# Kernel tuning notes

Measured on AMD Instinct MI355X. Metric: run time of the kernel, lower is better.

Reference implementation:

```python
import jax, jax.numpy as jnp
import numpy as np

N = 262144          # flattened node batch
IN_S, IN_V = 256, 32
OUT_S, OUT_V = 256, 32
H = max(IN_V, OUT_V)  # 32
EPS = 1e-4


def setup_inputs() -> dict:
    key = jax.random.key(0)
    ks = jax.random.split(key, 8)
    inv = lambda f: 1.0 / np.sqrt(f).astype(np.float32)
    return {
        "s": jax.random.normal(ks[0], (N, IN_S), jnp.float32),
        "V": jax.random.normal(ks[1], (N, IN_V, 3), jnp.float32),
        "W_h": jax.random.normal(ks[2], (H, IN_V), jnp.float32) * inv(IN_V),
        "W_mu": jax.random.normal(ks[3], (OUT_V, H), jnp.float32) * inv(H),
        "W_m_w": jax.random.normal(ks[4], (OUT_S, H + IN_S), jnp.float32) * inv(H + IN_S),
        "W_m_b": jax.random.normal(ks[5], (OUT_S,), jnp.float32) * 0.01,
        "W_g_w": jax.random.normal(ks[6], (OUT_V, OUT_S), jnp.float32) * inv(OUT_S),
        "W_g_b": jax.random.normal(ks[7], (OUT_V,), jnp.float32) * 0.01,
    }


def reference(s, V, W_h, W_mu, W_m_w, W_m_b, W_g_w, W_g_b):
    # V_h = W_h @ V : [N, H, 3]
    V_h = jnp.einsum('hv,nvc->nhc', W_h, V)
    # per-row L2 norm, clipped at eps : [N, H]
    s_h = jnp.maximum(jnp.linalg.norm(V_h, axis=-1), EPS)
    # Linear on concatenated scalars : [N, OUT_S]
    s_m = jnp.concatenate([s, s_h], axis=-1) @ W_m_w.T + W_m_b
    s_dash = jax.nn.relu(s_m)                      # sigma = relu
    # V_mu = W_mu @ V_h : [N, OUT_V, 3]
    V_mu = jnp.einsum('mh,nhc->nmc', W_mu, V_h)
    # vector gate: sigmoid(W_g(sigmoid(s_m)))  (sigma_plus = sigmoid)
    gate = jax.nn.sigmoid(jax.nn.sigmoid(s_m) @ W_g_w.T + W_g_b)  # [N, OUT_V]
    V_dash = gate[..., None] * V_mu
    return s_dash, V_dash
```

## Files before the change

### kernel.cpp

```cpp
#include <hip/hip_runtime.h>

#define NTOT 262144
#define BN   32
#define NT   256
#define SXS  296
#define VTS  36

typedef __attribute__((ext_vector_type(8))) short bf16x8;
typedef __attribute__((ext_vector_type(4))) float f32x4;

static __device__ __forceinline__ unsigned short f2b(float x) {
    union { float f; unsigned u; } c; c.f = x;
    unsigned r = c.u + 0x7FFFu + ((c.u >> 16) & 1u);
    return (unsigned short)(r >> 16);
}
static __device__ __forceinline__ float b2f(unsigned short h) {
    union { unsigned u; float f; } c; c.u = ((unsigned)h) << 16; return c.f;
}
static __device__ __forceinline__ bf16x8 cvt8(const float* p) {
    float4 x = *(const float4*)p, y = *(const float4*)(p + 4);
    bf16x8 r;
    r[0] = (short)f2b(x.x); r[1] = (short)f2b(x.y); r[2] = (short)f2b(x.z); r[3] = (short)f2b(x.w);
    r[4] = (short)f2b(y.x); r[5] = (short)f2b(y.y); r[6] = (short)f2b(y.z); r[7] = (short)f2b(y.w);
    return r;
}
static __device__ __forceinline__ void glds16(const unsigned short* g, void* l) {
    __builtin_amdgcn_global_load_lds(
        (const __attribute__((address_space(1))) void*)g,
        (__attribute__((address_space(3))) void*)l, 16, 0, 0);
}

__global__ void pack_w(const float* __restrict__ Wmw, const float* __restrict__ Wgw,
                       unsigned short* __restrict__ wp) {
    int t = blockIdx.x * 256 + threadIdx.x;
    if (t < 73728) {
        int o = t / 288, k = t % 288;
        int kks = (k & 31) ^ (((o >> 1) & 3) << 3);
        wp[(k >> 5) * 8192 + o * 32 + kks] = f2b(Wmw[t]);
    } else if (t < 81920) {
        int j = t - 73728;
        int o = j >> 8, k = j & 255;
        wp[73728 + (k >> 5) * 1024 + o * 32 + (k & 31)] = f2b(Wgw[j]);
    }
}

template<int USE_WS>
__global__ __launch_bounds__(NT, 2)
void gvp_main(const float* __restrict__ s, const float* __restrict__ V,
              const float* __restrict__ Wh, const float* __restrict__ Wmu,
              const float* __restrict__ Wmw, const float* __restrict__ Wmb,
              const float* __restrict__ Wgw, const float* __restrict__ Wgb,
              const unsigned short* __restrict__ wpack,
              float* __restrict__ out)
{
    __shared__ __attribute__((aligned(16))) unsigned short sX[BN * SXS];
    __shared__ __attribute__((aligned(16))) unsigned short sWb[2 * 8192];
    __shared__ __attribute__((aligned(16))) unsigned short sVT[96 * VTS];

    const int t  = threadIdx.x;
    const int w  = t >> 6, l = t & 63;
    const int fr = l & 15, fq = l >> 4;
    const int n0 = blockIdx.x * BN;
    const int half = w & 1, oh = w >> 1;

    if (USE_WS) {
        #pragma unroll
        for (int i = 0; i < 4; ++i)
            glds16(wpack + (w * 4 + i) * 512 + l * 8,
                   (char*)sWb + (w * 4 + i) * 1024);
    }

    #pragma unroll
    for (int i = 0; i < 8; ++i) {
        int n = i * 4 + w;
        float4 x4 = *(const float4*)&s[(size_t)(n0 + n) * 256 + 4 * l];
        ushort4 h4; h4.x = f2b(x4.x); h4.y = f2b(x4.y); h4.z = f2b(x4.z); h4.w = f2b(x4.w);
        *(ushort4*)&sX[n * SXS + 4 * l] = h4;
    }
    #pragma unroll
    for (int i = 0; i < 3; ++i) {
        int f = i * NT + t;
        float4 v4 = *(const float4*)&V[(size_t)n0 * 96 + f * 4];
        #pragma unroll
        for (int e = 0; e < 4; ++e) {
            int g = f * 4 + e;
            int n = g / 96, rem = g % 96, v = rem / 3, c = rem % 3;
            float val = (e == 0) ? v4.x : (e == 1) ? v4.y : (e == 2) ? v4.z : v4.w;
            sVT[(c * 32 + n) * VTS + v] = f2b(val);
        }
    }
    if (!USE_WS) {
        const float* p = &Wmw[t * 288];
        #pragma unroll
        for (int j = 0; j < 4; ++j)
            *(bf16x8*)&sWb[t * 32 + ((j ^ ((t >> 1) & 3)) << 3)] = cvt8(p + j * 8);
    }
    __syncthreads();

    {
        bf16x8 bh = cvt8(&Wh[(oh * 16 + fr) * 32 + fq * 8]);
        f32x4 va0 = {0,0,0,0}, va1 = {0,0,0,0}, va2 = {0,0,0,0};
        bf16x8 a0 = *(const bf16x8*)&sVT[(0 * 32 + half * 16 + fr) * VTS + fq * 8];
        bf16x8 a1 = *(const bf16x8*)&sVT[(1 * 32 + half * 16 + fr) * VTS + fq * 8];
        bf16x8 a2 = *(const bf16x8*)&sVT[(2 * 32 + half * 16 + fr) * VTS + fq * 8];
        va0 = __builtin_amdgcn_mfma_f32_16x16x32_bf16(a0, bh, va0, 0, 0, 0);
        va1 = __builtin_amdgcn_mfma_f32_16x16x32_bf16(a1, bh, va1, 0, 0, 0);
        va2 = __builtin_amdgcn_mfma_f32_16x16x32_bf16(a2, bh, va2, 0, 0, 0);
        __syncthreads();
        #pragma unroll
        for (int r = 0; r < 4; ++r) {
            int nl = half * 16 + fq * 4 + r;
            int h  = oh * 16 + fr;
            sVT[(0 * 32 + nl) * VTS + h] = f2b(va0[r]);
            sVT[(1 * 32 + nl) * VTS + h] = f2b(va1[r]);
            sVT[(2 * 32 + nl) * VTS + h] = f2b(va2[r]);
            float nrm = sqrtf(fmaf(va0[r], va0[r], fmaf(va1[r], va1[r], va2[r] * va2[r])));
            sX[nl * SXS + 256 + h] = f2b(fmaxf(nrm, 1e-4f));
        }
    }
    __syncthreads();

    f32x4 acc[2][4];
    #pragma unroll
    for (int mt = 0; mt < 2; ++mt)
        #pragma unroll
        for (int j = 0; j < 4; ++j) acc[mt][j] = (f32x4){0.f, 0.f, 0.f, 0.f};

    #pragma unroll
    for (int ks = 0; ks < 9; ++ks) {
        unsigned short* bw = sWb + (ks & 1) * 8192;
        if (USE_WS) {
            if (ks < 8) {
                #pragma unroll
                for (int i = 0; i < 4; ++i)
                    glds16(wpack + (ks + 1) * 8192 + (w * 4 + i) * 512 + l * 8,
                           (char*)sWb + ((ks + 1) & 1) * 16384 + (w * 4 + i) * 1024);
            }
        } else {
            bw = sWb;
            if (ks > 0) {
                __syncthreads();
                const float* p = &Wmw[t * 288 + ks * 32];
                #pragma unroll
                for (int j = 0; j < 4; ++j)
                    *(bf16x8*)&sWb[t * 32 + ((j ^ ((t >> 1) & 3)) << 3)] = cvt8(p + j * 8);
                __syncthreads();
            }
        }
        bf16x8 a0 = *(const bf16x8*)&sX[fr * SXS + ks * 32 + fq * 8];
        bf16x8 a1 = *(const bf16x8*)&sX[(16 + fr) * SXS + ks * 32 + fq * 8];
        bf16x8 b[4];
        #pragma unroll
        for (int j = 0; j < 4; ++j) {
            int o = w * 64 + j * 16 + fr;
            b[j] = *(const bf16x8*)&bw[o * 32 + ((fq * 8) ^ (((o >> 1) & 3) << 3))];
        }
        #pragma unroll
        for (int j = 0; j < 4; ++j) {
            acc[0][j] = __builtin_amdgcn_mfma_f32_16x16x32_bf16(a0, b[j], acc[0][j], 0, 0, 0);
            acc[1][j] = __builtin_amdgcn_mfma_f32_16x16x32_bf16(a1, b[j], acc[1][j], 0, 0, 0);
        }
        if (USE_WS) __syncthreads();
    }
    if (!USE_WS) __syncthreads();

    float bias[4];
    #pragma unroll
    for (int j = 0; j < 4; ++j) bias[j] = Wmb[w * 64 + j * 16 + fr];

    float* sRel = (float*)sWb;
    #pragma unroll
    for (int mt = 0; mt < 2; ++mt) {
        #pragma unroll
        for (int r = 0; r < 4; ++r) {
            int row  = fq * 4 + r;
            int node = mt * 16 + row;
            #pragma unroll
            for (int j = 0; j < 4; ++j) {
                int col = w * 64 + j * 16 + fr;
                float m = acc[mt][j][r] + bias[j];
                sX[node * SXS + col] = f2b(1.f / (1.f + __expf(-m)));
                sRel[row * 256 + col] = fmaxf(m, 0.f);
            }
        }
        __syncthreads();
        #pragma unroll
        for (int i = 0; i < 4; ++i) {
            int flat = i * NT + t;
            int row = flat >> 6, c4 = flat & 63;
            float4 v4 = *(const float4*)&sRel[row * 256 + c4 * 4];
            *(float4*)&out[(size_t)(n0 + mt * 16 + row) * 256 + c4 * 4] = v4;
        }
        __syncthreads();
    }

    {
        const int gmt = w & 1, gnt = w >> 1;
        f32x4 g = (f32x4){0.f, 0.f, 0.f, 0.f};
        #pragma unroll
        for (int ks = 0; ks < 8; ++ks) {
            bf16x8 a = *(const bf16x8*)&sX[(gmt * 16 + fr) * SXS + ks * 32 + fq * 8];
            bf16x8 b;
            if (USE_WS) b = *(const bf16x8*)&wpack[73728 + ks * 1024 + (gnt * 16 + fr) * 32 + fq * 8];
            else        b = cvt8(&Wgw[(gnt * 16 + fr) * 256 + ks * 32 + fq * 8]);
            g = __builtin_amdgcn_mfma_f32_16x16x32_bf16(a, b, g, 0, 0, 0);
        }
        int mo = gnt * 16 + fr;
        float gb = Wgb[mo];
        #pragma unroll
        for (int r = 0; r < 4; ++r) {
            int node = gmt * 16 + fq * 4 + r;
            sX[node * SXS + 256 + mo] = f2b(1.f / (1.f + __expf(-(g[r] + gb))));
        }
    }
    __syncthreads();

    float* sc = (float*)sWb;
    {
        bf16x8 bm = cvt8(&Wmu[(oh * 16 + fr) * 32 + fq * 8]);
        f32x4 m0 = {0,0,0,0}, m1 = {0,0,0,0}, m2 = {0,0,0,0};
        bf16x8 a0 = *(const bf16x8*)&sVT[(0 * 32 + half * 16 + fr) * VTS + fq * 8];
        bf16x8 a1 = *(const bf16x8*)&sVT[(1 * 32 + half * 16 + fr) * VTS + fq * 8];
        bf16x8 a2 = *(const bf16x8*)&sVT[(2 * 32 + half * 16 + fr) * VTS + fq * 8];
        m0 = __builtin_amdgcn_mfma_f32_16x16x32_bf16(a0, bm, m0, 0, 0, 0);
        m1 = __builtin_amdgcn_mfma_f32_16x16x32_bf16(a1, bm, m1, 0, 0, 0);
        m2 = __builtin_amdgcn_mfma_f32_16x16x32_bf16(a2, bm, m2, 0, 0, 0);
        #pragma unroll
        for (int r = 0; r < 4; ++r) {
            int node = half * 16 + fq * 4 + r;
            int m    = oh * 16 + fr;
            float g  = b2f(sX[node * SXS + 256 + m]);
            sc[node * 96 + m * 3 + 0] = g * m0[r];
            sc[node * 96 + m * 3 + 1] = g * m1[r];
            sc[node * 96 + m * 3 + 2] = g * m2[r];
        }
    }
    __syncthreads();
    const size_t VBASE = (size_t)NTOT * 256;
    #pragma unroll
    for (int i = 0; i < 3; ++i) {
        int f = i * NT + t;
        *(float4*)&out[VBASE + (size_t)n0 * 96 + f * 4] = *(const float4*)&sc[f * 4];
    }
}

extern "C" void kernel_launch(void* const* d_in, const int* in_sizes, int n_in,
                              void* d_out, int out_size, void* d_ws, size_t ws_size,
                              hipStream_t stream) {
    const float* s   = (const float*)d_in[0];
    const float* V   = (const float*)d_in[1];
    const float* Wh  = (const float*)d_in[2];
    const float* Wmu = (const float*)d_in[3];
    const float* Wmw = (const float*)d_in[4];
    const float* Wmb = (const float*)d_in[5];
    const float* Wgw = (const float*)d_in[6];
    const float* Wgb = (const float*)d_in[7];
    float* out = (float*)d_out;

    dim3 grid(NTOT / BN);
    dim3 block(NT);

    if (ws_size >= 163840) {
        pack_w<<<320, 256, 0, stream>>>(Wmw, Wgw, (unsigned short*)d_ws);
        gvp_main<1><<<grid, block, 0, stream>>>(s, V, Wh, Wmu, Wmw, Wmb, Wgw, Wgb,
                                                (const unsigned short*)d_ws, out);
    } else {
        gvp_main<0><<<grid, block, 0, stream>>>(s, V, Wh, Wmu, Wmw, Wmb, Wgw, Wgb,
                                                nullptr, out);
    }
}
```

Before: 251.8 us.

## Halve weight LDS buffer via 128-column chunks, raise occupancy, vectorize V transpose

Splits the W_m weight staging into 128-output-column chunks so each double-buffered LDS slice is half the size, repacking the global weight layout and reordering accumulator column mapping to match. The reduced shared memory allows raising launch bounds to three blocks per SM. It also rewrites the V transpose load so each thread loads 12 contiguous floats and writes three ushort4s instead of per-element scatter with divisions. The trade-off is twice as many K-loop iterations and barriers, plus tighter register budget at higher occupancy.

```diff
diff --git a/kernel.cpp b/kernel.cpp
--- a/kernel.cpp
+++ b/kernel.cpp
@@ -35,8 +35,9 @@
     int t = blockIdx.x * 256 + threadIdx.x;
     if (t < 73728) {
         int o = t / 288, k = t % 288;
-        int kks = (k & 31) ^ (((o >> 1) & 3) << 3);
-        wp[(k >> 5) * 8192 + o * 32 + kks] = f2b(Wmw[t]);
+        int ks = k >> 5, kk = k & 31, ch = o >> 7, ol = o & 127;
+        int kks = kk ^ (((ol >> 1) & 3) << 3);
+        wp[(ks * 2 + ch) * 4096 + ol * 32 + kks] = f2b(Wmw[t]);
     } else if (t < 81920) {
         int j = t - 73728;
         int o = j >> 8, k = j & 255;
@@ -45,7 +46,7 @@
 }
 
 template<int USE_WS>
-__global__ __launch_bounds__(NT, 2)
+__global__ __launch_bounds__(NT, 3)
 void gvp_main(const float* __restrict__ s, const float* __restrict__ V,
               const float* __restrict__ Wh, const float* __restrict__ Wmu,
               const float* __restrict__ Wmw, const float* __restrict__ Wmb,
@@ -54,7 +55,7 @@
               float* __restrict__ out)
 {
     __shared__ __attribute__((aligned(16))) unsigned short sX[BN * SXS];
-    __shared__ __attribute__((aligned(16))) unsigned short sWb[2 * 8192];
+    __shared__ __attribute__((aligned(16))) unsigned short sWb[2 * 4096];
     __shared__ __attribute__((aligned(16))) unsigned short sVT[96 * VTS];
 
     const int t  = threadIdx.x;
@@ -64,10 +65,10 @@
     const int half = w & 1, oh = w >> 1;
 
     if (USE_WS) {
-        #pragma unroll
-        for (int i = 0; i < 4; ++i)
-            glds16(wpack + (w * 4 + i) * 512 + l * 8,
-                   (char*)sWb + (w * 4 + i) * 1024);
+        const unsigned short* src = wpack + w * 1024 + l * 8;
+        unsigned short* dst = sWb + w * 1024;
+        glds16(src, dst);
+        glds16(src + 512, dst + 512);
     }
 
     #pragma unroll
@@ -77,23 +78,24 @@
         ushort4 h4; h4.x = f2b(x4.x); h4.y = f2b(x4.y); h4.z = f2b(x4.z); h4.w = f2b(x4.w);
         *(ushort4*)&sX[n * SXS + 4 * l] = h4;
     }
-    #pragma unroll
-    for (int i = 0; i < 3; ++i) {
-        int f = i * NT + t;
-        float4 v4 = *(const float4*)&V[(size_t)n0 * 96 + f * 4];
-        #pragma unroll
-        for (int e = 0; e < 4; ++e) {
-            int g = f * 4 + e;
-            int n = g / 96, rem = g % 96, v = rem / 3, c = rem % 3;
-            float val = (e == 0) ? v4.x : (e == 1) ? v4.y : (e == 2) ? v4.z : v4.w;
-            sVT[(c * 32 + n) * VTS + v] = f2b(val);
-        }
+    {
+        int n = t >> 3, vq = t & 7;
+        const float* p = &V[(size_t)(n0 + n) * 96 + vq * 12];
+        float4 q0 = *(const float4*)(p);
+        float4 q1 = *(const float4*)(p + 4);
+        float4 q2 = *(const float4*)(p + 8);
+        ushort4 c0 = { f2b(q0.x), f2b(q0.w), f2b(q1.z), f2b(q2.y) };
+        ushort4 c1 = { f2b(q0.y), f2b(q1.x), f2b(q1.w), f2b(q2.z) };
+        ushort4 c2 = { f2b(q0.z), f2b(q1.y), f2b(q2.x), f2b(q2.w) };
+        *(ushort4*)&sVT[(0 * 32 + n) * VTS + vq * 4] = c0;
+        *(ushort4*)&sVT[(1 * 32 + n) * VTS + vq * 4] = c1;
+        *(ushort4*)&sVT[(2 * 32 + n) * VTS + vq * 4] = c2;
     }
     if (!USE_WS) {
-        const float* p = &Wmw[t * 288];
-        #pragma unroll
-        for (int j = 0; j < 4; ++j)
-            *(bf16x8*)&sWb[t * 32 + ((j ^ ((t >> 1) & 3)) << 3)] = cvt8(p + j * 8);
+        int ol = w * 32 + (l >> 1), kh = l & 1, x = (ol >> 1) & 3;
+        const float* p = &Wmw[ol * 288 + kh * 16];
+        *(bf16x8*)&sWb[ol * 32 + (((kh * 2 + 0) ^ x) << 3)] = cvt8(p);
+        *(bf16x8*)&sWb[ol * 32 + (((kh * 2 + 1) ^ x) << 3)] = cvt8(p + 8);
     }
     __syncthreads();
 
@@ -126,47 +128,45 @@
         #pragma unroll
         for (int j = 0; j < 4; ++j) acc[mt][j] = (f32x4){0.f, 0.f, 0.f, 0.f};
 
-    #pragma unroll
-    for (int ks = 0; ks < 9; ++ks) {
-        unsigned short* bw = sWb + (ks & 1) * 8192;
-        if (USE_WS) {
-            if (ks < 8) {
-                #pragma unroll
-                for (int i = 0; i < 4; ++i)
-                    glds16(wpack + (ks + 1) * 8192 + (w * 4 + i) * 512 + l * 8,
-                           (char*)sWb + ((ks + 1) & 1) * 16384 + (w * 4 + i) * 1024);
+    const int ol0 = w * 32 + fr, ol1 = ol0 + 16;
+    const int bo0 = ol0 * 32 + ((fq ^ ((ol0 >> 1) & 3)) << 3);
+    const int bo1 = ol1 * 32 + ((fq ^ ((ol1 >> 1) & 3)) << 3);
+
+    #pragma unroll
+    for (int it = 0; it < 18; ++it) {
+        if (it < 17) {
+            if (USE_WS) {
+                const unsigned short* src = wpack + (it + 1) * 4096 + w * 1024 + l * 8;
+                unsigned short* dst = sWb + ((it + 1) & 1) * 4096 + w * 1024;
+                glds16(src, dst);
+                glds16(src + 512, dst + 512);
+            } else {
+                int it1 = it + 1, ks1 = it1 >> 1, ch1 = it1 & 1;
+                int ol = w * 32 + (l >> 1), kh = l & 1, x = (ol >> 1) & 3;
+                const float* p = &Wmw[(ch1 * 128 + ol) * 288 + ks1 * 32 + kh * 16];
+                unsigned short* dst = sWb + (it1 & 1) * 4096;
+                *(bf16x8*)&dst[ol * 32 + (((kh * 2 + 0) ^ x) << 3)] = cvt8(p);
+                *(bf16x8*)&dst[ol * 32 + (((kh * 2 + 1) ^ x) << 3)] = cvt8(p + 8);
             }
-        } else {
-            bw = sWb;
-            if (ks > 0) {
-                __syncthreads();
-                const float* p = &Wmw[t * 288 + ks * 32];
-                #pragma unroll
-                for (int j = 0; j < 4; ++j)
-                    *(bf16x8*)&sWb[t * 32 + ((j ^ ((t >> 1) & 3)) << 3)] = cvt8(p + j * 8);
-                __syncthreads();
-            }
-        }
+        }
+        const int ks = it >> 1;
+        const unsigned short* bw = sWb + (it & 1) * 4096;
         bf16x8 a0 = *(const bf16x8*)&sX[fr * SXS + ks * 32 + fq * 8];
         bf16x8 a1 = *(const bf16x8*)&sX[(16 + fr) * SXS + ks * 32 + fq * 8];
-        bf16x8 b[4];
-        #pragma unroll
-        for (int j = 0; j < 4; ++j) {
-            int o = w * 64 + j * 16 + fr;
-            b[j] = *(const bf16x8*)&bw[o * 32 + ((fq * 8) ^ (((o >> 1) & 3) << 3))];
-        }
-        #pragma unroll
-        for (int j = 0; j < 4; ++j) {
-            acc[0][j] = __builtin_amdgcn_mfma_f32_16x16x32_bf16(a0, b[j], acc[0][j], 0, 0, 0);
-            acc[1][j] = __builtin_amdgcn_mfma_f32_16x16x32_bf16(a1, b[j], acc[1][j], 0, 0, 0);
-        }
-        if (USE_WS) __syncthreads();
-    }
-    if (!USE_WS) __syncthreads();
+        bf16x8 b0 = *(const bf16x8*)&bw[bo0];
+        bf16x8 b1 = *(const bf16x8*)&bw[bo1];
+        const int ji = (it & 1) * 2;
+        acc[0][ji + 0] = __builtin_amdgcn_mfma_f32_16x16x32_bf16(a0, b0, acc[0][ji + 0], 0, 0, 0);
+        acc[1][ji + 0] = __builtin_amdgcn_mfma_f32_16x16x32_bf16(a1, b0, acc[1][ji + 0], 0, 0, 0);
+        acc[0][ji + 1] = __builtin_amdgcn_mfma_f32_16x16x32_bf16(a0, b1, acc[0][ji + 1], 0, 0, 0);
+        acc[1][ji + 1] = __builtin_amdgcn_mfma_f32_16x16x32_bf16(a1, b1, acc[1][ji + 1], 0, 0, 0);
+        __syncthreads();
+    }
 
     float bias[4];
     #pragma unroll
-    for (int j = 0; j < 4; ++j) bias[j] = Wmb[w * 64 + j * 16 + fr];
+    for (int ji = 0; ji < 4; ++ji)
+        bias[ji] = Wmb[(ji >> 1) * 128 + w * 32 + (ji & 1) * 16 + fr];
 
     float* sRel = (float*)sWb;
     #pragma unroll
@@ -176,9 +176,9 @@
             int row  = fq * 4 + r;
             int node = mt * 16 + row;
             #pragma unroll
-            for (int j = 0; j < 4; ++j) {
-                int col = w * 64 + j * 16 + fr;
-                float m = acc[mt][j][r] + bias[j];
+            for (int ji = 0; ji < 4; ++ji) {
+                int col = (ji >> 1) * 128 + w * 32 + (ji & 1) * 16 + fr;
+                float m = acc[mt][ji][r] + bias[ji];
                 sX[node * SXS + col] = f2b(1.f / (1.f + __expf(-m)));
                 sRel[row * 256 + col] = fmaxf(m, 0.f);
             }
```

Result: faster. 219.6 us (-12.8%).
